# Kernel tuning notes

Hardware: AMD Instinct MI355X
Metric: run time of the kernel (lower is better)

Reference implementation:

```python
import jax, jax.numpy as jnp
import numpy as np

D_MODEL = 1024
H = 16
D_K = D_MODEL // H
B = 2
S = 2048


def setup_inputs() -> dict:
    key = jax.random.key(0)
    ks = jax.random.split(key, 11)
    scale = 1.0 / np.sqrt(D_MODEL)
    inp = {
        "query": jax.random.normal(ks[0], (B, S, D_MODEL), jnp.float32),
        "key_in": jax.random.normal(ks[1], (B, S, D_MODEL), jnp.float32),
        "value": jax.random.normal(ks[2], (B, S, D_MODEL), jnp.float32),
        # causal mask, broadcast over heads: 1 = keep, 0 = masked
        "mask": jnp.tril(jnp.ones((S, S), jnp.int32))[None, None, :, :].repeat(B, axis=0),
        "w_q": jax.random.normal(ks[3], (D_MODEL, D_MODEL), jnp.float32) * scale,
        "b_q": jax.random.normal(ks[4], (D_MODEL,), jnp.float32) * 0.01,
        "w_k": jax.random.normal(ks[5], (D_MODEL, D_MODEL), jnp.float32) * scale,
        "b_k": jax.random.normal(ks[6], (D_MODEL,), jnp.float32) * 0.01,
        "w_v": jax.random.normal(ks[7], (D_MODEL, D_MODEL), jnp.float32) * scale,
        "b_v": jax.random.normal(ks[8], (D_MODEL,), jnp.float32) * 0.01,
        "w_out": jax.random.normal(ks[9], (D_MODEL, D_MODEL), jnp.float32) * scale,
        "b_out": jax.random.normal(ks[10], (D_MODEL,), jnp.float32) * 0.01,
    }
    return inp


def _split_heads(x):
    # [B,S,D] -> [B,H,S,d_k]
    b, s, _ = x.shape
    return x.reshape(b, s, H, D_K).transpose(0, 2, 1, 3)


def reference(query, key_in, value, mask, w_q, b_q, w_k, b_k, w_v, b_v, w_out, b_out):
    q = _split_heads(query @ w_q.T + b_q)
    k = _split_heads(key_in @ w_k.T + b_k)
    v = _split_heads(value @ w_v.T + b_v)
    scores = jnp.einsum("bhqd,bhkd->bhqk", q, k) / jnp.sqrt(jnp.float32(D_K))
    scores = jnp.where(mask == 0, jnp.float32(-1e9), scores)
    attn = jax.nn.softmax(scores, axis=-1)  # dropout rate 0.0 -> identity
    out = jnp.einsum("bhqk,bhkd->bhqd", attn, v)
    out = out.transpose(0, 2, 1, 3).reshape(query.shape[0], -1, D_MODEL)
    return out @ w_out.T + b_out
```

## Files before the change

kernel.cpp:

```cpp
#include <hip/hip_runtime.h>
#include <hip/hip_bf16.h>

#define D_MODEL 1024
#define NH 16
#define DKH 64
#define BB 2
#define SS 2048
#define MTOT (BB * SS)

typedef __hip_bfloat16 bf16;
typedef __attribute__((ext_vector_type(8))) short short8;
typedef __attribute__((ext_vector_type(4))) short short4v;
typedef __attribute__((ext_vector_type(4))) float floatx4;

__device__ __forceinline__ bf16 f2bf(float x) { return __float2bfloat16(x); }

__device__ __forceinline__ void async_cp16(const void* g, void* l) {
  __builtin_amdgcn_global_load_lds(
      (const __attribute__((address_space(1))) unsigned int*)g,
      (__attribute__((address_space(3))) unsigned int*)l, 16, 0, 0);
}

__global__ __launch_bounds__(256) void convert_kernel(
    const float* __restrict__ wq, const float* __restrict__ wk,
    const float* __restrict__ wv, const float* __restrict__ wo,
    const float* __restrict__ qi, const float* __restrict__ ki,
    const float* __restrict__ vi, bf16* __restrict__ Wb,
    bf16* __restrict__ Qi, bf16* __restrict__ Ki, bf16* __restrict__ Vi) {
  const int id = blockIdx.x * 256 + threadIdx.x;
  const float* src;
  bf16* dst;
  if (id < (1 << 20)) {
    const int m = id >> 18, loc = id & 0x3FFFF;
    src = ((m == 0) ? wq : (m == 1) ? wk : (m == 2) ? wv : wo) + (size_t)loc * 4;
    dst = Wb + ((size_t)m << 20) + (size_t)loc * 4;
  } else {
    const int t = id - (1 << 20);
    const int m = t >> 20, loc = t & 0xFFFFF;
    src = ((m == 0) ? qi : (m == 1) ? ki : vi) + (size_t)loc * 4;
    dst = ((m == 0) ? Qi : (m == 1) ? Ki : Vi) + (size_t)loc * 4;
  }
  const float4 v = *(const float4*)src;
  short4v s;
  bf16* pb = (bf16*)&s;
  pb[0] = f2bf(v.x); pb[1] = f2bf(v.y); pb[2] = f2bf(v.z); pb[3] = f2bf(v.w);
  *(short4v*)dst = s;
}

__device__ __forceinline__ void gemm_qkv_body(const bf16* __restrict__ A,
                                              const bf16* __restrict__ W,
                                              const float* __restrict__ Bi,
                                              bf16* __restrict__ C, int mode) {
  constexpr int N = 1024, K = 1024;
  __shared__ bf16 As[2][128 * 32];
  __shared__ bf16 Ws[2][128 * 32];

  const int tid = threadIdx.x;
  const int w = tid >> 6, lane = tid & 63, quad = lane >> 4, n16 = lane & 15;
  const int bx = blockIdx.x;
  const int bm = bx & 31, bn = bx >> 5;
  const int wm = (w & 1) * 64, wn = (w >> 1) * 64;

  const int rb = lane >> 2, cb = lane & 3;
  const int gsw = (cb ^ ((rb >> 1) & 3)) * 8;
  const int rkey = ((n16 >> 1) & 3) * 8;

  const bf16* Ag0 = A + (size_t)(bm * 128) * K;
  const bf16* Wg0 = W + (size_t)(bn * 128) * K;

  auto issue = [&](int buf, int k0) {
#pragma unroll
    for (int ii = 0; ii < 2; ii++) {
      const int R = w * 32 + ii * 16 + rb;
      async_cp16(Ag0 + (size_t)R * K + k0 + gsw,
                 (void*)&As[buf][(w * 32 + ii * 16) * 32]);
      async_cp16(Wg0 + (size_t)R * K + k0 + gsw,
                 (void*)&Ws[buf][(w * 32 + ii * 16) * 32]);
    }
  };

  floatx4 acc[4][4] = {};
  issue(0, 0);
  int buf = 0;
  for (int k0 = 0; k0 < K; k0 += 32) {
    __syncthreads();
    if (k0 + 32 < K) issue(buf ^ 1, k0 + 32);

    short8 af[4], bfr[4];
#pragma unroll
    for (int i = 0; i < 4; i++)
      af[i] = *(const short8*)(&As[buf][(wm + i * 16 + n16) * 32 + ((quad * 8) ^ rkey)]);
#pragma unroll
    for (int j = 0; j < 4; j++)
      bfr[j] = *(const short8*)(&Ws[buf][(wn + j * 16 + n16) * 32 + ((quad * 8) ^ rkey)]);
#pragma unroll
    for (int i = 0; i < 4; i++)
#pragma unroll
      for (int j = 0; j < 4; j++)
        acc[i][j] = __builtin_amdgcn_mfma_f32_16x16x32_bf16(af[i], bfr[j], acc[i][j], 0, 0, 0);
    buf ^= 1;
  }

  float bv[4];
#pragma unroll
  for (int j = 0; j < 4; j++) bv[j] = Bi[bn * 128 + wn + j * 16 + n16];

#pragma unroll
  for (int i = 0; i < 4; i++) {
    const int rowb = bm * 128 + wm + i * 16 + quad * 4;
#pragma unroll
    for (int j = 0; j < 4; j++) {
      const int col = bn * 128 + wn + j * 16 + n16;
      if (mode == 1) {
        short4v s;
        bf16* pb = (bf16*)&s;
#pragma unroll
        for (int r = 0; r < 4; r++) pb[r] = f2bf(acc[i][j][r] + bv[j]);
        *(short4v*)(C + (size_t)col * MTOT + rowb) = s;
      } else {
#pragma unroll
        for (int r = 0; r < 4; r++)
          C[(size_t)(rowb + r) * N + col] = f2bf(acc[i][j][r] + bv[j]);
      }
    }
  }
}

__global__ __launch_bounds__(256) void gemm_qkv_kernel(
    const bf16* __restrict__ Qi, const bf16* __restrict__ Ki,
    const bf16* __restrict__ Vi, const bf16* __restrict__ Wb,
    const float* __restrict__ bq, const float* __restrict__ bk,
    const float* __restrict__ bv, bf16* __restrict__ Qw,
    bf16* __restrict__ Kw, bf16* __restrict__ VTw) {
  const int z = blockIdx.z;
  const bf16* A = (z == 0) ? Qi : (z == 1) ? Ki : Vi;
  const bf16* W = Wb + ((size_t)z << 20);
  const float* Bi = (z == 0) ? bq : (z == 1) ? bk : bv;
  bf16* C = (z == 0) ? Qw : (z == 1) ? Kw : VTw;
  gemm_qkv_body(A, W, Bi, C, (z == 2) ? 1 : 0);
}

__global__ __launch_bounds__(256) void gemm_out_kernel(
    const bf16* __restrict__ A, const bf16* __restrict__ W,
    const float* __restrict__ Bi, float* __restrict__ C) {
  constexpr int N = 1024, K = 1024;
  __shared__ bf16 As[2][128 * 32];
  __shared__ bf16 Ws[2][64 * 32];

  const int tid = threadIdx.x;
  const int w = tid >> 6, lane = tid & 63, quad = lane >> 4, n16 = lane & 15;
  const int bx = blockIdx.x;
  const int bm = bx & 31, bn = bx >> 5;
  const int wm = w * 32;

  const int rb = lane >> 2, cb = lane & 3;
  const int gsw = (cb ^ ((rb >> 1) & 3)) * 8;
  const int rkey = ((n16 >> 1) & 3) * 8;

  const bf16* Ag0 = A + (size_t)(bm * 128) * K;
  const bf16* Wg0 = W + (size_t)(bn * 64) * K;

  auto issue = [&](int buf, int kk) {
#pragma unroll
    for (int ii = 0; ii < 2; ii++) {
      const int R = w * 32 + ii * 16 + rb;
      async_cp16(Ag0 + (size_t)R * K + kk + gsw,
                 (void*)&As[buf][(w * 32 + ii * 16) * 32]);
    }
    const int Rw = w * 16 + rb;
    async_cp16(Wg0 + (size_t)Rw * K + kk + gsw, (void*)&Ws[buf][(w * 16) * 32]);
  };

  floatx4 acc[2][4] = {};
  issue(0, 0);
  int buf = 0;
  for (int k0 = 0; k0 < K; k0 += 32) {
    __syncthreads();
    if (k0 + 32 < K) issue(buf ^ 1, k0 + 32);

    short8 af[2], bfr[4];
#pragma unroll
    for (int i = 0; i < 2; i++)
      af[i] = *(const short8*)(&As[buf][(wm + i * 16 + n16) * 32 + ((quad * 8) ^ rkey)]);
#pragma unroll
    for (int j = 0; j < 4; j++)
      bfr[j] = *(const short8*)(&Ws[buf][(j * 16 + n16) * 32 + ((quad * 8) ^ rkey)]);
#pragma unroll
    for (int i = 0; i < 2; i++)
#pragma unroll
      for (int j = 0; j < 4; j++)
        acc[i][j] = __builtin_amdgcn_mfma_f32_16x16x32_bf16(af[i], bfr[j], acc[i][j], 0, 0, 0);
    buf ^= 1;
  }

  float bv[4];
#pragma unroll
  for (int j = 0; j < 4; j++) bv[j] = Bi[bn * 64 + j * 16 + n16];

#pragma unroll
  for (int i = 0; i < 2; i++) {
    const int rowb = bm * 128 + wm + i * 16 + quad * 4;
#pragma unroll
    for (int j = 0; j < 4; j++) {
      const int col = bn * 64 + j * 16 + n16;
#pragma unroll
      for (int r = 0; r < 4; r++)
        C[(size_t)(rowb + r) * N + col] = acc[i][j][r] + bv[j];
    }
  }
}

__global__ __launch_bounds__(256, 4) void attn_kernel(const bf16* __restrict__ Q,
                                                      const bf16* __restrict__ Kg,
                                                      const bf16* __restrict__ VT,
                                                      bf16* __restrict__ O) {
  constexpr int BN = 64;
  __shared__ bf16 Ks[2][64 * 64];
  __shared__ bf16 Vs[2][64 * 64];
  __shared__ bf16 Pw[4][16 * 64];

  const int tid = threadIdx.x;
  const int w = tid >> 6, lane = tid & 63, quad = lane >> 4, n16 = lane & 15;
  const int hb = blockIdx.x;
  const int h = hb & 15, b = hb >> 4;
  const int q0 = (31 - (int)blockIdx.y) * 64;
  const size_t qoff = (size_t)b * SS * D_MODEL + h * DKH;
  const bf16* VTh = VT + (size_t)(h * DKH) * MTOT + (size_t)b * SS;

  const int kvr = tid >> 3, ck = tid & 7;
  const int wkey = (kvr & 7) << 3;
  const int swz = (n16 & 7) << 3;

  short8 kreg[2], vreg[2];
  auto loadKV = [&](int kv0) {
#pragma unroll
    for (int ii = 0; ii < 2; ii++) {
      kreg[ii] = *(const short8*)(Kg + qoff + (size_t)(kv0 + ii * 32 + kvr) * D_MODEL + ck * 8);
      vreg[ii] = *(const short8*)(VTh + (size_t)(ii * 32 + kvr) * MTOT + kv0 + ck * 8);
    }
  };

  bf16* pwb = &Pw[w][0];
  const int q0w = q0 + w * 16;
  const int nt = q0 / 64 + 1;

  short8 aQ0, aQ1;
  {
    const bf16* qp = Q + qoff + (size_t)(q0w + n16) * D_MODEL + quad * 8;
    aQ0 = *(const short8*)(qp);
    aQ1 = *(const short8*)(qp + 32);
  }

  floatx4 facc[4] = {};
  float lsum = 0.f;

  loadKV(0);
  int buf = 0;
  for (int t = 0; t < nt; t++) {
#pragma unroll
    for (int ii = 0; ii < 2; ii++) {
      *(short8*)(&Ks[buf][(ii * 32 + kvr) * 64 + ((ck * 8) ^ wkey)]) = kreg[ii];
      *(short8*)(&Vs[buf][(ii * 32 + kvr) * 64 + ((ck * 8) ^ wkey)]) = vreg[ii];
    }
    if (t + 1 < nt) loadKV((t + 1) * BN);
    __syncthreads();

    const int kv0 = t * BN;
    const bool lastT = (t == nt - 1);
    const bf16* ksb = &Ks[buf][0];

#pragma unroll
    for (int blk = 0; blk < 4; blk++) {
      const int krow = blk * 16 + n16;
      short8 ak0 = *(const short8*)(ksb + krow * 64 + ((quad * 8) ^ swz));
      short8 ak1 = *(const short8*)(ksb + krow * 64 + ((quad * 8 + 32) ^ swz));
      floatx4 z = {};
      z = __builtin_amdgcn_mfma_f32_16x16x32_bf16(ak0, aQ0, z, 0, 0, 0);
      z = __builtin_amdgcn_mfma_f32_16x16x32_bf16(ak1, aQ1, z, 0, 0, 0);
      short4v s;
      bf16* pb = (bf16*)&s;
      if (lastT) {
        const int kbase = kv0 + blk * 16 + quad * 4, qcol = q0w + n16;
#pragma unroll
        for (int r = 0; r < 4; r++) {
          float pe = __expf(z[r] * 0.125f);
          if (kbase + r > qcol) pe = 0.f;
          lsum += pe;
          pb[r] = f2bf(pe);
        }
      } else {
#pragma unroll
        for (int r = 0; r < 4; r++) {
          const float pe = __expf(z[r] * 0.125f);
          lsum += pe;
          pb[r] = f2bf(pe);
        }
      }
      *(short4v*)(pwb + n16 * 64 + ((blk * 16 + quad * 4) ^ swz)) = s;
    }

    short8 aP[2];
#pragma unroll
    for (int c = 0; c < 2; c++)
      aP[c] = *(const short8*)(pwb + n16 * 64 + ((c * 32 + quad * 8) ^ swz));

    const bf16* vsb = &Vs[buf][0];
    __builtin_amdgcn_s_setprio(1);
#pragma unroll
    for (int d = 0; d < 4; d++)
#pragma unroll
      for (int c = 0; c < 2; c++) {
        short8 bvf = *(const short8*)(vsb + (d * 16 + n16) * 64 + ((c * 32 + quad * 8) ^ swz));
        facc[d] = __builtin_amdgcn_mfma_f32_16x16x32_bf16(aP[c], bvf, facc[d], 0, 0, 0);
      }
    __builtin_amdgcn_s_setprio(0);
    buf ^= 1;
  }

  lsum += __shfl_xor(lsum, 16);
  lsum += __shfl_xor(lsum, 32);
#pragma unroll
  for (int r = 0; r < 4; r++) {
    const float linv = 1.f / __shfl(lsum, quad * 4 + r);
    const int qrow = q0w + quad * 4 + r;
    bf16* op = O + qoff + (size_t)qrow * D_MODEL;
#pragma unroll
    for (int d = 0; d < 4; d++) op[d * 16 + n16] = f2bf(facc[d][r] * linv);
  }
}

extern "C" void kernel_launch(void* const* d_in, const int* in_sizes, int n_in,
                              void* d_out, int out_size, void* d_ws, size_t ws_size,
                              hipStream_t stream) {
  (void)in_sizes; (void)n_in; (void)out_size; (void)ws_size;
  const float* query  = (const float*)d_in[0];
  const float* key_in = (const float*)d_in[1];
  const float* value  = (const float*)d_in[2];
  const float* w_q = (const float*)d_in[4];
  const float* b_q = (const float*)d_in[5];
  const float* w_k = (const float*)d_in[6];
  const float* b_k = (const float*)d_in[7];
  const float* w_v = (const float*)d_in[8];
  const float* b_v = (const float*)d_in[9];
  const float* w_o = (const float*)d_in[10];
  const float* b_o = (const float*)d_in[11];
  float* outp = (float*)d_out;

  const size_t mat = (size_t)MTOT * D_MODEL;
  bf16* Qws  = (bf16*)d_ws;
  bf16* Kws  = Qws + mat;
  bf16* VTws = Kws + mat;
  bf16* Wb   = VTws + mat;
  bf16* Vi   = Wb + 4 * (size_t)(1 << 20);
  bf16* Qi = (bf16*)d_out;
  bf16* Ki = Qi + mat;

  convert_kernel<<<16384, 256, 0, stream>>>(w_q, w_k, w_v, w_o, query, key_in,
                                            value, Wb, Qi, Ki, Vi);

  dim3 gq(256, 1, 3);
  gemm_qkv_kernel<<<gq, 256, 0, stream>>>(Qi, Ki, Vi, Wb, b_q, b_k, b_v, Qws,
                                          Kws, VTws);
  dim3 ga(NH * BB, 32);
  attn_kernel<<<ga, 256, 0, stream>>>(Qws, Kws, VTws, Qws);
  gemm_out_kernel<<<512, 256, 0, stream>>>(Qws, Wb + ((size_t)3 << 20), b_o, outp);
}
```

Measured before the change: 230.4 us.

## Enlarge QKV GEMM tiles to 256x256 with 3-stage async pipeline

Rewrites the QKV projection GEMM to use 256x256 block tiles with 512 threads (8 waves, 128x64 per wave), a triple-buffered LDS pipeline with explicit vmcnt waits instead of __syncthreads, and s_setprio around the MFMA block. The aim is more data reuse per tile and better overlap of global loads with compute. The trade-off is only 192 blocks for 256 CUs, which leaves some CUs idle, plus higher register and LDS pressure (96KB LDS).

```diff
diff --git a/kernel.cpp b/kernel.cpp
--- a/kernel.cpp
+++ b/kernel.cpp
@@ -47,97 +47,115 @@
   *(short4v*)dst = s;
 }
 
-__device__ __forceinline__ void gemm_qkv_body(const bf16* __restrict__ A,
-                                              const bf16* __restrict__ W,
-                                              const float* __restrict__ Bi,
-                                              bf16* __restrict__ C, int mode) {
-  constexpr int N = 1024, K = 1024;
-  __shared__ bf16 As[2][128 * 32];
-  __shared__ bf16 Ws[2][128 * 32];
-
-  const int tid = threadIdx.x;
-  const int w = tid >> 6, lane = tid & 63, quad = lane >> 4, n16 = lane & 15;
-  const int bx = blockIdx.x;
-  const int bm = bx & 31, bn = bx >> 5;
-  const int wm = (w & 1) * 64, wn = (w >> 1) * 64;
-
-  const int rb = lane >> 2, cb = lane & 3;
-  const int gsw = (cb ^ ((rb >> 1) & 3)) * 8;
-  const int rkey = ((n16 >> 1) & 3) * 8;
-
-  const bf16* Ag0 = A + (size_t)(bm * 128) * K;
-  const bf16* Wg0 = W + (size_t)(bn * 128) * K;
-
-  auto issue = [&](int buf, int k0) {
-#pragma unroll
-    for (int ii = 0; ii < 2; ii++) {
-      const int R = w * 32 + ii * 16 + rb;
-      async_cp16(Ag0 + (size_t)R * K + k0 + gsw,
-                 (void*)&As[buf][(w * 32 + ii * 16) * 32]);
-      async_cp16(Wg0 + (size_t)R * K + k0 + gsw,
-                 (void*)&Ws[buf][(w * 32 + ii * 16) * 32]);
-    }
-  };
-
-  floatx4 acc[4][4] = {};
-  issue(0, 0);
-  int buf = 0;
-  for (int k0 = 0; k0 < K; k0 += 32) {
-    __syncthreads();
-    if (k0 + 32 < K) issue(buf ^ 1, k0 + 32);
-
-    short8 af[4], bfr[4];
-#pragma unroll
-    for (int i = 0; i < 4; i++)
-      af[i] = *(const short8*)(&As[buf][(wm + i * 16 + n16) * 32 + ((quad * 8) ^ rkey)]);
-#pragma unroll
-    for (int j = 0; j < 4; j++)
-      bfr[j] = *(const short8*)(&Ws[buf][(wn + j * 16 + n16) * 32 + ((quad * 8) ^ rkey)]);
-#pragma unroll
-    for (int i = 0; i < 4; i++)
-#pragma unroll
-      for (int j = 0; j < 4; j++)
-        acc[i][j] = __builtin_amdgcn_mfma_f32_16x16x32_bf16(af[i], bfr[j], acc[i][j], 0, 0, 0);
-    buf ^= 1;
-  }
-
-  float bv[4];
-#pragma unroll
-  for (int j = 0; j < 4; j++) bv[j] = Bi[bn * 128 + wn + j * 16 + n16];
-
-#pragma unroll
-  for (int i = 0; i < 4; i++) {
-    const int rowb = bm * 128 + wm + i * 16 + quad * 4;
-#pragma unroll
-    for (int j = 0; j < 4; j++) {
-      const int col = bn * 128 + wn + j * 16 + n16;
-      if (mode == 1) {
-        short4v s;
-        bf16* pb = (bf16*)&s;
-#pragma unroll
-        for (int r = 0; r < 4; r++) pb[r] = f2bf(acc[i][j][r] + bv[j]);
-        *(short4v*)(C + (size_t)col * MTOT + rowb) = s;
-      } else {
-#pragma unroll
-        for (int r = 0; r < 4; r++)
-          C[(size_t)(rowb + r) * N + col] = f2bf(acc[i][j][r] + bv[j]);
-      }
-    }
-  }
-}
-
-__global__ __launch_bounds__(256) void gemm_qkv_kernel(
+__global__ __launch_bounds__(512, 2) void gemm_qkv_kernel(
     const bf16* __restrict__ Qi, const bf16* __restrict__ Ki,
     const bf16* __restrict__ Vi, const bf16* __restrict__ Wb,
     const float* __restrict__ bq, const float* __restrict__ bk,
     const float* __restrict__ bv, bf16* __restrict__ Qw,
     bf16* __restrict__ Kw, bf16* __restrict__ VTw) {
+  constexpr int N = 1024, K = 1024, NT = K / 32;
+  __shared__ bf16 As[3][256 * 32];
+  __shared__ bf16 Ws[3][256 * 32];
+
   const int z = blockIdx.z;
   const bf16* A = (z == 0) ? Qi : (z == 1) ? Ki : Vi;
   const bf16* W = Wb + ((size_t)z << 20);
   const float* Bi = (z == 0) ? bq : (z == 1) ? bk : bv;
-  bf16* C = (z == 0) ? Qw : (z == 1) ? Kw : VTw;
-  gemm_qkv_body(A, W, Bi, C, (z == 2) ? 1 : 0);
+
+  const int tid = threadIdx.x;
+  const int wid = tid >> 6, lane = tid & 63, quad = lane >> 4, n16 = lane & 15;
+  const int wr = wid >> 2, wc = wid & 3;
+  const int bx = blockIdx.x;
+  const int bm = bx & 15, bn = bx >> 4;
+
+  const int rb = lane >> 2, cb = lane & 3;
+  const int gsw = (cb ^ ((rb >> 1) & 3)) * 8;
+  const int rkey = ((n16 >> 1) & 3) * 8;
+
+  const bf16* Ag0 = A + (size_t)(bm * 256) * K;
+  const bf16* Wg0 = W + (size_t)(bn * 256) * K;
+
+  auto issue = [&](int buf, int k0) {
+#pragma unroll
+    for (int ii = 0; ii < 2; ii++) {
+      const int R = wid * 32 + ii * 16 + rb;
+      async_cp16(Ag0 + (size_t)R * K + k0 + gsw,
+                 (void*)&As[buf][(wid * 32 + ii * 16) * 32]);
+      async_cp16(Wg0 + (size_t)R * K + k0 + gsw,
+                 (void*)&Ws[buf][(wid * 32 + ii * 16) * 32]);
+    }
+  };
+
+  floatx4 acc[8][4] = {};
+  issue(0, 0);
+  issue(1, 32);
+  int cur = 0;
+  for (int t = 0; t < NT; t++) {
+    if (t < NT - 1) {
+      asm volatile("s_waitcnt vmcnt(4)" ::: "memory");
+    } else {
+      asm volatile("s_waitcnt vmcnt(0)" ::: "memory");
+    }
+    __builtin_amdgcn_s_barrier();
+    __builtin_amdgcn_sched_barrier(0);
+
+    if (t < NT - 2) {
+      int nb = cur + 2;
+      if (nb >= 3) nb -= 3;
+      issue(nb, (t + 2) * 32);
+    }
+
+    short8 af[8], bfr[4];
+#pragma unroll
+    for (int i = 0; i < 8; i++)
+      af[i] = *(const short8*)(&As[cur][(wr * 128 + i * 16 + n16) * 32 + ((quad * 8) ^ rkey)]);
+#pragma unroll
+    for (int j = 0; j < 4; j++)
+      bfr[j] = *(const short8*)(&Ws[cur][(wc * 64 + j * 16 + n16) * 32 + ((quad * 8) ^ rkey)]);
+
+    __builtin_amdgcn_s_setprio(1);
+#pragma unroll
+    for (int i = 0; i < 8; i++)
+#pragma unroll
+      for (int j = 0; j < 4; j++)
+        acc[i][j] = __builtin_amdgcn_mfma_f32_16x16x32_bf16(af[i], bfr[j], acc[i][j], 0, 0, 0);
+    __builtin_amdgcn_s_setprio(0);
+
+    cur = (cur == 2) ? 0 : cur + 1;
+  }
+
+  float bvv[4];
+#pragma unroll
+  for (int j = 0; j < 4; j++) bvv[j] = Bi[bn * 256 + wc * 64 + j * 16 + n16];
+
+  if (z == 2) {
+#pragma unroll
+    for (int i = 0; i < 8; i++) {
+      const int rowb = bm * 256 + wr * 128 + i * 16 + quad * 4;
+#pragma unroll
+      for (int j = 0; j < 4; j++) {
+        const int col = bn * 256 + wc * 64 + j * 16 + n16;
+        short4v s;
+        bf16* pb = (bf16*)&s;
+#pragma unroll
+        for (int r = 0; r < 4; r++) pb[r] = f2bf(acc[i][j][r] + bvv[j]);
+        *(short4v*)(VTw + (size_t)col * MTOT + rowb) = s;
+      }
+    }
+  } else {
+    bf16* C = (z == 0) ? Qw : Kw;
+#pragma unroll
+    for (int i = 0; i < 8; i++) {
+      const int rowb = bm * 256 + wr * 128 + i * 16 + quad * 4;
+#pragma unroll
+      for (int j = 0; j < 4; j++) {
+        const int col = bn * 256 + wc * 64 + j * 16 + n16;
+#pragma unroll
+        for (int r = 0; r < 4; r++)
+          C[(size_t)(rowb + r) * N + col] = f2bf(acc[i][j][r] + bvv[j]);
+      }
+    }
+  }
 }
 
 __global__ __launch_bounds__(256) void gemm_out_kernel(
@@ -358,8 +376,8 @@
   convert_kernel<<<16384, 256, 0, stream>>>(w_q, w_k, w_v, w_o, query, key_in,
                                             value, Wb, Qi, Ki, Vi);
 
-  dim3 gq(256, 1, 3);
-  gemm_qkv_kernel<<<gq, 256, 0, stream>>>(Qi, Ki, Vi, Wb, b_q, b_k, b_v, Qws,
+  dim3 gq(64, 1, 3);
+  gemm_qkv_kernel<<<gq, 512, 0, stream>>>(Qi, Ki, Vi, Wb, b_q, b_k, b_v, Qws,
                                           Kws, VTws);
   dim3 ga(NH * BB, 32);
   attn_kernel<<<ga, 256, 0, stream>>>(Qws, Kws, VTws, Qws);
```

Result: slower. 239.6 us (+4.0%).

## Triple-buffer GEMM LDS loads with partial vmcnt waits; relax attention barrier

Applied to the files above, without the earlier changes.

Both projection GEMMs move from double to triple buffering of the async global-to-LDS copies, issuing loads two tiles ahead. Each iteration waits only on the older tile using an explicit partial s_waitcnt vmcnt, so one prefetch can stay in flight across the barrier. The attention loop's __syncthreads is replaced by an LDS-only wait plus a raw barrier, so the barrier no longer waits on the outstanding global K/V register loads. This uses more LDS per block, which may cut occupancy, and correctness now depends on the hand-counted vmcnt values matching the number of issued loads.

```diff
diff --git a/kernel.cpp b/kernel.cpp
--- a/kernel.cpp
+++ b/kernel.cpp
@@ -51,9 +51,9 @@
                                               const bf16* __restrict__ W,
                                               const float* __restrict__ Bi,
                                               bf16* __restrict__ C, int mode) {
-  constexpr int N = 1024, K = 1024;
-  __shared__ bf16 As[2][128 * 32];
-  __shared__ bf16 Ws[2][128 * 32];
+  constexpr int N = 1024, K = 1024, NT = K / 32;
+  __shared__ bf16 As[3][128 * 32];
+  __shared__ bf16 Ws[3][128 * 32];
 
   const int tid = threadIdx.x;
   const int w = tid >> 6, lane = tid & 63, quad = lane >> 4, n16 = lane & 15;
@@ -81,24 +81,37 @@
 
   floatx4 acc[4][4] = {};
   issue(0, 0);
-  int buf = 0;
-  for (int k0 = 0; k0 < K; k0 += 32) {
-    __syncthreads();
-    if (k0 + 32 < K) issue(buf ^ 1, k0 + 32);
+  issue(1, 32);
+  int cur = 0;
+  for (int t = 0; t < NT; t++) {
+    if (t < NT - 1) {
+      asm volatile("s_waitcnt vmcnt(4)" ::: "memory");
+    } else {
+      asm volatile("s_waitcnt vmcnt(0)" ::: "memory");
+    }
+    __builtin_amdgcn_s_barrier();
+    __builtin_amdgcn_sched_barrier(0);
+
+    if (t < NT - 2) {
+      int nb = cur + 2;
+      if (nb >= 3) nb -= 3;
+      issue(nb, (t + 2) * 32);
+    }
 
     short8 af[4], bfr[4];
 #pragma unroll
     for (int i = 0; i < 4; i++)
-      af[i] = *(const short8*)(&As[buf][(wm + i * 16 + n16) * 32 + ((quad * 8) ^ rkey)]);
+      af[i] = *(const short8*)(&As[cur][(wm + i * 16 + n16) * 32 + ((quad * 8) ^ rkey)]);
 #pragma unroll
     for (int j = 0; j < 4; j++)
-      bfr[j] = *(const short8*)(&Ws[buf][(wn + j * 16 + n16) * 32 + ((quad * 8) ^ rkey)]);
+      bfr[j] = *(const short8*)(&Ws[cur][(wn + j * 16 + n16) * 32 + ((quad * 8) ^ rkey)]);
 #pragma unroll
     for (int i = 0; i < 4; i++)
 #pragma unroll
       for (int j = 0; j < 4; j++)
         acc[i][j] = __builtin_amdgcn_mfma_f32_16x16x32_bf16(af[i], bfr[j], acc[i][j], 0, 0, 0);
-    buf ^= 1;
+
+    cur = (cur == 2) ? 0 : cur + 1;
   }
 
   float bv[4];
@@ -143,9 +156,9 @@
 __global__ __launch_bounds__(256) void gemm_out_kernel(
     const bf16* __restrict__ A, const bf16* __restrict__ W,
     const float* __restrict__ Bi, float* __restrict__ C) {
-  constexpr int N = 1024, K = 1024;
-  __shared__ bf16 As[2][128 * 32];
-  __shared__ bf16 Ws[2][64 * 32];
+  constexpr int N = 1024, K = 1024, NT = K / 32;
+  __shared__ bf16 As[3][128 * 32];
+  __shared__ bf16 Ws[3][64 * 32];
 
   const int tid = threadIdx.x;
   const int w = tid >> 6, lane = tid & 63, quad = lane >> 4, n16 = lane & 15;
@@ -173,24 +186,37 @@
 
   floatx4 acc[2][4] = {};
   issue(0, 0);
-  int buf = 0;
-  for (int k0 = 0; k0 < K; k0 += 32) {
-    __syncthreads();
-    if (k0 + 32 < K) issue(buf ^ 1, k0 + 32);
+  issue(1, 32);
+  int cur = 0;
+  for (int t = 0; t < NT; t++) {
+    if (t < NT - 1) {
+      asm volatile("s_waitcnt vmcnt(3)" ::: "memory");
+    } else {
+      asm volatile("s_waitcnt vmcnt(0)" ::: "memory");
+    }
+    __builtin_amdgcn_s_barrier();
+    __builtin_amdgcn_sched_barrier(0);
+
+    if (t < NT - 2) {
+      int nb = cur + 2;
+      if (nb >= 3) nb -= 3;
+      issue(nb, (t + 2) * 32);
+    }
 
     short8 af[2], bfr[4];
 #pragma unroll
     for (int i = 0; i < 2; i++)
-      af[i] = *(const short8*)(&As[buf][(wm + i * 16 + n16) * 32 + ((quad * 8) ^ rkey)]);
+      af[i] = *(const short8*)(&As[cur][(wm + i * 16 + n16) * 32 + ((quad * 8) ^ rkey)]);
 #pragma unroll
     for (int j = 0; j < 4; j++)
-      bfr[j] = *(const short8*)(&Ws[buf][(j * 16 + n16) * 32 + ((quad * 8) ^ rkey)]);
+      bfr[j] = *(const short8*)(&Ws[cur][(j * 16 + n16) * 32 + ((quad * 8) ^ rkey)]);
 #pragma unroll
     for (int i = 0; i < 2; i++)
 #pragma unroll
       for (int j = 0; j < 4; j++)
         acc[i][j] = __builtin_amdgcn_mfma_f32_16x16x32_bf16(af[i], bfr[j], acc[i][j], 0, 0, 0);
-    buf ^= 1;
+
+    cur = (cur == 2) ? 0 : cur + 1;
   }
 
   float bv[4];
@@ -263,7 +289,9 @@
       *(short8*)(&Vs[buf][(ii * 32 + kvr) * 64 + ((ck * 8) ^ wkey)]) = vreg[ii];
     }
     if (t + 1 < nt) loadKV((t + 1) * BN);
-    __syncthreads();
+    asm volatile("s_waitcnt lgkmcnt(0)" ::: "memory");
+    __builtin_amdgcn_s_barrier();
+    __builtin_amdgcn_sched_barrier(0);
 
     const int kv0 = t * BN;
     const bool lastT = (t == nt - 1);
```

New measurement: 223.4 us. 1.03x faster.
